# Performance work log

Hardware: AMD Instinct MI355X
Metric: run time of the kernel (lower is better)

## Reference

```python
import jax, jax.numpy as jnp
import numpy as np

LN_EPS = 1e-5


def setup_inputs() -> dict:
    key = jax.random.key(0)
    k1, k2, k3 = jax.random.split(key, 3)
    B, L, D = 8, 2048, 512
    K, Dc = 8192, 16
    x = jax.random.normal(k1, (B, L, D), dtype=jnp.float32)
    # xavier_uniform for Linear(dim -> codebook_dim), weight shape (Dc, D)
    bound = float(np.sqrt(6.0 / (D + Dc)))
    proj_weight = jax.random.uniform(k2, (Dc, D), dtype=jnp.float32, minval=-bound, maxval=bound)
    codebook = jax.random.normal(k3, (K, Dc), dtype=jnp.float32)
    return {"x": x, "proj_weight": proj_weight, "codebook": codebook}


def reference(x, proj_weight, codebook):
    # random projection: (B,L,D) @ (D,Dc) -> (B,L,Dc)
    h = jnp.einsum("bld,cd->blc", x, proj_weight)
    # LayerNorm over last dim, no affine params
    mu = jnp.mean(h, axis=-1, keepdims=True)
    var = jnp.mean(jnp.square(h - mu), axis=-1, keepdims=True)
    h = (h - mu) / jnp.sqrt(var + LN_EPS)
    # squared-distance via dot-product decomposition; avoids (B,L,K,Dc) blowup.
    # argmin of ||h - c||^2 == argmin of ||h - c|| (sqrt is monotone).
    h2 = jnp.sum(jnp.square(h), axis=-1, keepdims=True)        # (B,L,1)
    c2 = jnp.sum(jnp.square(codebook), axis=-1)                # (K,)
    dots = jnp.einsum("blc,kc->blk", h, codebook)              # (B,L,K)
    dist2 = h2 - 2.0 * dots + c2                               # (B,L,K)
    codes = jnp.argmin(dist2, axis=-1)                         # (B,L) int
    return codes
```

## Files before the change

kernel.cpp:

```cpp
#include <hip/hip_runtime.h>
#include <math.h>

#define LN_EPS 1e-5f

typedef _Float16 f16;
typedef _Float16 f16x8 __attribute__((ext_vector_type(8)));
typedef _Float16 f16x2 __attribute__((ext_vector_type(2)));
typedef float f32x4 __attribute__((ext_vector_type(4)));
typedef unsigned long long ull;

constexpr int DC = 16;
constexpr int K = 8192;
constexpr int NTOK = 16384;
constexpr int KSPLIT = 16;
constexpr int KCHUNK = K / KSPLIT;
constexpr int JT = 8;
constexpr float SCALE = 16384.f;
constexpr float EPS_S = LN_EPS * SCALE * SCALE;
constexpr int XP = 516;

__global__ __launch_bounds__(256, 4) void prep_proj(
    const float* __restrict__ x, const float* __restrict__ wq,
    const float* __restrict__ cb, f16* __restrict__ hB,
    f16* __restrict__ cbA, float* __restrict__ c2s) {
  const int tid = threadIdx.x;

  if (blockIdx.x >= NTOK / 16) {
    const int ti = tid >> 6;
    const int l = tid & 63;
    const int ct = (blockIdx.x - NTOK / 16) * 4 + ti;
    const int code = ct * 16 + (l & 15);
    const int g = l >> 4;

    const float* row = cb + (size_t)code * DC + (g & 1) * 8;
    f32x4 v0 = *(const f32x4*)row;
    f32x4 v1 = *(const f32x4*)(row + 4);
    float vv[8] = {v0[0], v0[1], v0[2], v0[3], v1[0], v1[1], v1[2], v1[3]};

    f16x8 r;
#pragma unroll
    for (int p = 0; p < 8; ++p) {
      float cc = -128.f * vv[p];
      f16 hh = (f16)cc;
      r[p] = (g < 2) ? hh : (f16)(cc - (float)hh);
    }
    *(f16x8*)(cbA + ((size_t)ct * 64 + l) * 8) = r;

    if (g == 0) {
      const f32x4* rw = (const f32x4*)(cb + (size_t)code * DC);
      f32x4 a0 = rw[0], a1 = rw[1], a2 = rw[2], a3 = rw[3];
      float s = 0.f;
#pragma unroll
      for (int p = 0; p < 4; ++p)
        s += a0[p] * a0[p] + a1[p] * a1[p] + a2[p] * a2[p] + a3[p] * a3[p];
      c2s[code] = (s + 16.5f) * SCALE;
    }
    return;
  }

  __shared__ float xs[16 * XP];
  __shared__ float comb[4 * 16 * 20];
  __shared__ float hsm[16][17];

  const float4* xg = (const float4*)(x + (size_t)blockIdx.x * (16 * 512));
#pragma unroll
  for (int i = 0; i < 8; ++i) {
    int idx = tid + 256 * i;
    int tok = idx >> 7;
    int d4 = idx & 127;
    *(float4*)&xs[tok * XP + d4 * 4] = xg[idx];
  }

  const int w = tid >> 6;
  const int lane = tid & 63;
  const int g = lane >> 4;
  const int c_out = lane & 15;
  const int doff = (g & 1) * 8;
  f16x8 aw[8];
#pragma unroll
  for (int st = 0; st < 8; ++st) {
    const int step = w * 8 + st;
    const float* wp = wq + (size_t)c_out * 512 + step * 16 + doff;
    f32x4 u0 = *(const f32x4*)wp;
    f32x4 u1 = *(const f32x4*)(wp + 4);
    float v[8] = {u0[0], u0[1], u0[2], u0[3], u1[0], u1[1], u1[2], u1[3]};
    f16x8 r;
#pragma unroll
    for (int p = 0; p < 8; ++p) {
      float f = v[p] * 64.f;
      f16 h1 = (f16)f;
      r[p] = (g < 2) ? h1 : (f16)(f - (float)h1);
    }
    aw[st] = r;
  }
  __syncthreads();

  f32x4 acc = {0.f, 0.f, 0.f, 0.f};
  const int tok = lane & 15;
#pragma unroll
  for (int st = 0; st < 8; ++st) {
    const int step = w * 8 + st;
    const float* xp = &xs[tok * XP + step * 16 + doff];
    f32x4 u0 = *(const f32x4*)xp;
    f32x4 u1 = *(const f32x4*)(xp + 4);
    float v[8] = {u0[0], u0[1], u0[2], u0[3], u1[0], u1[1], u1[2], u1[3]};
    f16x8 bh, bl;
#pragma unroll
    for (int p = 0; p < 8; ++p) {
      float f = v[p] * 256.f;
      f16 h1 = (f16)f;
      bh[p] = h1;
      bl[p] = (f16)(f - (float)h1);
    }
    f16x8 b1 = (g < 2) ? bh : bl;
    f16x8 b2 = (g < 2) ? bl : bh;
    acc = __builtin_amdgcn_mfma_f32_16x16x32_f16(aw[st], b1, acc, 0, 0, 0);
    acc = __builtin_amdgcn_mfma_f32_16x16x32_f16(aw[st], b2, acc, 0, 0, 0);
  }

  *(f32x4*)&comb[w * 320 + tok * 20 + g * 4] = acc;
  __syncthreads();

  const int tokL = tid >> 4;
  const int cL = tid & 15;
  float hv = (comb[0 * 320 + tokL * 20 + cL] + comb[1 * 320 + tokL * 20 + cL]) +
             (comb[2 * 320 + tokL * 20 + cL] + comb[3 * 320 + tokL * 20 + cL]);

  float s = hv;
  s += __shfl_xor(s, 1, 16);
  s += __shfl_xor(s, 2, 16);
  s += __shfl_xor(s, 4, 16);
  s += __shfl_xor(s, 8, 16);
  float mu = s * (1.f / 16.f);
  float diff = hv - mu;
  float v2 = diff * diff;
  v2 += __shfl_xor(v2, 1, 16);
  v2 += __shfl_xor(v2, 2, 16);
  v2 += __shfl_xor(v2, 4, 16);
  v2 += __shfl_xor(v2, 8, 16);
  float var = v2 * (1.f / 16.f);
  hsm[tokL][cL] = diff / sqrtf(var + EPS_S);
  __syncthreads();

  const int le = tid >> 2;
  const int q = tid & 3;
  const int col = le & 15;
  const int ge = le >> 4;
  const int s0 = ge * 8 + q * 2;
  f16x2 u;
#pragma unroll
  for (int e = 0; e < 2; ++e) {
    int sE = s0 + e;
    int d = sE & 15;
    float f = hsm[col][d] * 256.f;
    f16 hh = (f16)f;
    u[e] = (sE < 16) ? hh : (f16)(f - (float)hh);
  }
  *(f16x2*)(hB + ((size_t)blockIdx.x * 64 + le) * 8 + q * 2) = u;
}

__global__ __launch_bounds__(256, 4) void argmin_mfma(
    const f16* __restrict__ cbA, const float* __restrict__ c2s,
    const f16* __restrict__ hB, ull* __restrict__ pk) {
  const int tid = threadIdx.x;
  const int w = tid >> 6;
  const int lane = tid & 63;
  const int kt0 = blockIdx.y * (KCHUNK / 16);
  const int tt0 = blockIdx.x * (4 * JT) + w * JT;

  f16x8 b1[JT], b2[JT];
#pragma unroll
  for (int j = 0; j < JT; ++j) {
    const f16* p = hB + ((size_t)(tt0 + j) * 64) * 8;
    b1[j] = *(const f16x8*)&p[lane * 8];
    b2[j] = *(const f16x8*)&p[(lane ^ 32) * 8];
  }

  float best[JT];
  int bidx[JT];
#pragma unroll
  for (int j = 0; j < JT; ++j) {
    best[j] = 3.0e38f;
    bidx[j] = 0;
  }

  const int lkoff = (lane >> 4) * 4;
#pragma unroll 2
  for (int t = 0; t < KCHUNK / 16; ++t) {
    f16x8 a = *(const f16x8*)&cbA[((size_t)(kt0 + t) * 64 + lane) * 8];
    const int kbase = blockIdx.y * KCHUNK + t * 16;
    f32x4 c2v = *(const f32x4*)&c2s[kbase + lkoff];
    const int ib = kbase + lkoff;
#pragma unroll
    for (int j = 0; j < JT; ++j) {
      f32x4 acc =
          __builtin_amdgcn_mfma_f32_16x16x32_f16(a, b1[j], c2v, 0, 0, 0);
      acc = __builtin_amdgcn_mfma_f32_16x16x32_f16(a, b2[j], acc, 0, 0, 0);
#pragma unroll
      for (int r = 0; r < 4; ++r) {
        bool lt = acc[r] < best[j];
        best[j] = lt ? acc[r] : best[j];
        bidx[j] = lt ? (ib + r) : bidx[j];
      }
    }
  }

#pragma unroll
  for (int j = 0; j < JT; ++j) {
    float d = best[j];
    int ix = bidx[j];
#pragma unroll
    for (int off = 16; off <= 32; off <<= 1) {
      float od = __shfl_xor(d, off);
      int oi = __shfl_xor(ix, off);
      bool take = (od < d) || (od == d && oi < ix);
      d = take ? od : d;
      ix = take ? oi : ix;
    }
    d = fmaxf(d, 0.f);
    if (lane < 16) {
      int token = (tt0 + j) * 16 + lane;
      ull key = ((ull)__float_as_uint(d) << 32) | (unsigned)ix;
      pk[(size_t)token * KSPLIT + blockIdx.y] = key;
    }
  }
}

__global__ __launch_bounds__(256) void finalize(const ull* __restrict__ pk,
                                                int* __restrict__ out) {
  int t = blockIdx.x * 256 + threadIdx.x;
  const ull* row = pk + (size_t)t * KSPLIT;
  ull best = row[0];
#pragma unroll
  for (int s = 1; s < KSPLIT; ++s) {
    ull k2 = row[s];
    best = (k2 < best) ? k2 : best;
  }
  out[t] = (int)(unsigned)(best & 0xFFFFFFFFull);
}

extern "C" void kernel_launch(void* const* d_in, const int* in_sizes, int n_in,
                              void* d_out, int out_size, void* d_ws,
                              size_t ws_size, hipStream_t stream) {
  const float* x = (const float*)d_in[0];
  const float* w = (const float*)d_in[1];
  const float* cb = (const float*)d_in[2];

  f16* cbA = (f16*)d_ws;
  float* c2s = (float*)(cbA + (size_t)K * 32);
  f16* hB = (f16*)(c2s + K);
  ull* pk = (ull*)(hB + (size_t)NTOK * 32);

  prep_proj<<<NTOK / 16 + K / 64, 256, 0, stream>>>(x, w, cb, hB, cbA, c2s);
  argmin_mfma<<<dim3(NTOK / (64 * JT), KSPLIT), 256, 0, stream>>>(cbA, c2s,
                                                                  hB, pk);
  finalize<<<NTOK / 256, 256, 0, stream>>>(pk, (int*)d_out);
}
```

Baseline: 48.29 us.

## Fuse projection, LayerNorm and codebook argmin into one kernel with exact rescoring

Replaces the three-kernel pipeline with a codebook-prep kernel plus one fused kernel. Each 1024-thread block projects and normalises 64 tokens, then scans the whole codebook, with each wave covering a slice of 512 codes. The fused kernel tracks only the best group of four codes per MFMA tile, reduces across waves in LDS, and rescores the four winning candidates exactly in fp32. This removes the hB and partial-key round trips through global memory, the finalize launch, and most per-element compare work. In exchange it runs fewer, larger blocks, reads x straight from global memory instead of staging it in LDS, and relies on the approximate group-level choice being correct.

```diff
diff --git a/kernel.cpp b/kernel.cpp
--- a/kernel.cpp
+++ b/kernel.cpp
@@ -5,82 +5,75 @@
 
 typedef _Float16 f16;
 typedef _Float16 f16x8 __attribute__((ext_vector_type(8)));
-typedef _Float16 f16x2 __attribute__((ext_vector_type(2)));
 typedef float f32x4 __attribute__((ext_vector_type(4)));
-typedef unsigned long long ull;
 
 constexpr int DC = 16;
 constexpr int K = 8192;
 constexpr int NTOK = 16384;
-constexpr int KSPLIT = 16;
-constexpr int KCHUNK = K / KSPLIT;
-constexpr int JT = 8;
+constexpr int D = 512;
 constexpr float SCALE = 16384.f;
 constexpr float EPS_S = LN_EPS * SCALE * SCALE;
-constexpr int XP = 516;
-
-__global__ __launch_bounds__(256, 4) void prep_proj(
+
+__global__ __launch_bounds__(256) void prep_cb(const float* __restrict__ cb,
+                                               f16* __restrict__ cbA,
+                                               float* __restrict__ c2s) {
+  const int tid = threadIdx.x;
+  const int ti = tid >> 6;
+  const int l = tid & 63;
+  const int ct = blockIdx.x * 4 + ti;
+  const int code = ct * 16 + (l & 15);
+  const int g = l >> 4;
+
+  const float* row = cb + (size_t)code * DC + (g & 1) * 8;
+  f32x4 v0 = *(const f32x4*)row;
+  f32x4 v1 = *(const f32x4*)(row + 4);
+  float vv[8] = {v0[0], v0[1], v0[2], v0[3], v1[0], v1[1], v1[2], v1[3]};
+
+  f16x8 r;
+#pragma unroll
+  for (int p = 0; p < 8; ++p) {
+    float cc = -128.f * vv[p];
+    f16 hh = (f16)cc;
+    r[p] = (g < 2) ? hh : (f16)(cc - (float)hh);
+  }
+  *(f16x8*)(cbA + ((size_t)ct * 64 + l) * 8) = r;
+
+  if (g == 0) {
+    const f32x4* rw = (const f32x4*)(cb + (size_t)code * DC);
+    f32x4 a0 = rw[0], a1 = rw[1], a2 = rw[2], a3 = rw[3];
+    float s = 0.f;
+#pragma unroll
+    for (int p = 0; p < 4; ++p)
+      s += a0[p] * a0[p] + a1[p] * a1[p] + a2[p] * a2[p] + a3[p] * a3[p];
+    c2s[code] = (s + 16.5f) * SCALE;
+  }
+}
+
+__global__ __launch_bounds__(1024, 4) void fused(
     const float* __restrict__ x, const float* __restrict__ wq,
-    const float* __restrict__ cb, f16* __restrict__ hB,
-    f16* __restrict__ cbA, float* __restrict__ c2s) {
+    const float* __restrict__ cb, const f16* __restrict__ cbA,
+    const float* __restrict__ c2s, int* __restrict__ out) {
+  __shared__ float comb[16 * 320];
+  __shared__ float hsm[64][17];
+  __shared__ float fin_d[16][64];
+  __shared__ int fin_t[16][64];
+
   const int tid = threadIdx.x;
-
-  if (blockIdx.x >= NTOK / 16) {
-    const int ti = tid >> 6;
-    const int l = tid & 63;
-    const int ct = (blockIdx.x - NTOK / 16) * 4 + ti;
-    const int code = ct * 16 + (l & 15);
-    const int g = l >> 4;
-
-    const float* row = cb + (size_t)code * DC + (g & 1) * 8;
-    f32x4 v0 = *(const f32x4*)row;
-    f32x4 v1 = *(const f32x4*)(row + 4);
-    float vv[8] = {v0[0], v0[1], v0[2], v0[3], v1[0], v1[1], v1[2], v1[3]};
-
-    f16x8 r;
-#pragma unroll
-    for (int p = 0; p < 8; ++p) {
-      float cc = -128.f * vv[p];
-      f16 hh = (f16)cc;
-      r[p] = (g < 2) ? hh : (f16)(cc - (float)hh);
-    }
-    *(f16x8*)(cbA + ((size_t)ct * 64 + l) * 8) = r;
-
-    if (g == 0) {
-      const f32x4* rw = (const f32x4*)(cb + (size_t)code * DC);
-      f32x4 a0 = rw[0], a1 = rw[1], a2 = rw[2], a3 = rw[3];
-      float s = 0.f;
-#pragma unroll
-      for (int p = 0; p < 4; ++p)
-        s += a0[p] * a0[p] + a1[p] * a1[p] + a2[p] * a2[p] + a3[p] * a3[p];
-      c2s[code] = (s + 16.5f) * SCALE;
-    }
-    return;
-  }
-
-  __shared__ float xs[16 * XP];
-  __shared__ float comb[4 * 16 * 20];
-  __shared__ float hsm[16][17];
-
-  const float4* xg = (const float4*)(x + (size_t)blockIdx.x * (16 * 512));
-#pragma unroll
-  for (int i = 0; i < 8; ++i) {
-    int idx = tid + 256 * i;
-    int tok = idx >> 7;
-    int d4 = idx & 127;
-    *(float4*)&xs[tok * XP + d4 * 4] = xg[idx];
-  }
-
   const int w = tid >> 6;
   const int lane = tid & 63;
   const int g = lane >> 4;
-  const int c_out = lane & 15;
+  const int col = lane & 15;
   const int doff = (g & 1) * 8;
+  const int tb = blockIdx.x * 64;
+
+  const int j = w & 3;
+  const int dq = w >> 2;
+
   f16x8 aw[8];
 #pragma unroll
   for (int st = 0; st < 8; ++st) {
-    const int step = w * 8 + st;
-    const float* wp = wq + (size_t)c_out * 512 + step * 16 + doff;
+    const int step = dq * 8 + st;
+    const float* wp = wq + (size_t)col * D + step * 16 + doff;
     f32x4 u0 = *(const f32x4*)wp;
     f32x4 u1 = *(const f32x4*)(wp + 4);
     float v[8] = {u0[0], u0[1], u0[2], u0[3], u1[0], u1[1], u1[2], u1[3]};
@@ -93,14 +86,13 @@
     }
     aw[st] = r;
   }
-  __syncthreads();
 
   f32x4 acc = {0.f, 0.f, 0.f, 0.f};
-  const int tok = lane & 15;
+  const float* xrow = x + (size_t)(tb + j * 16 + col) * D;
 #pragma unroll
   for (int st = 0; st < 8; ++st) {
-    const int step = w * 8 + st;
-    const float* xp = &xs[tok * XP + step * 16 + doff];
+    const int step = dq * 8 + st;
+    const float* xp = xrow + step * 16 + doff;
     f32x4 u0 = *(const f32x4*)xp;
     f32x4 u1 = *(const f32x4*)(xp + 4);
     float v[8] = {u0[0], u0[1], u0[2], u0[3], u1[0], u1[1], u1[2], u1[3]};
@@ -117,15 +109,17 @@
     acc = __builtin_amdgcn_mfma_f32_16x16x32_f16(aw[st], b1, acc, 0, 0, 0);
     acc = __builtin_amdgcn_mfma_f32_16x16x32_f16(aw[st], b2, acc, 0, 0, 0);
   }
-
-  *(f32x4*)&comb[w * 320 + tok * 20 + g * 4] = acc;
+  *(f32x4*)&comb[w * 320 + col * 20 + g * 4] = acc;
   __syncthreads();
 
   const int tokL = tid >> 4;
   const int cL = tid & 15;
-  float hv = (comb[0 * 320 + tokL * 20 + cL] + comb[1 * 320 + tokL * 20 + cL]) +
-             (comb[2 * 320 + tokL * 20 + cL] + comb[3 * 320 + tokL * 20 + cL]);
-
+  const int jL = tokL >> 4;
+  const int colL = tokL & 15;
+  float hv = (comb[(0 * 4 + jL) * 320 + colL * 20 + cL] +
+              comb[(1 * 4 + jL) * 320 + colL * 20 + cL]) +
+             (comb[(2 * 4 + jL) * 320 + colL * 20 + cL] +
+              comb[(3 * 4 + jL) * 320 + colL * 20 + cL]);
   float s = hv;
   s += __shfl_xor(s, 1, 16);
   s += __shfl_xor(s, 2, 16);
@@ -142,101 +136,98 @@
   hsm[tokL][cL] = diff / sqrtf(var + EPS_S);
   __syncthreads();
 
-  const int le = tid >> 2;
-  const int q = tid & 3;
-  const int col = le & 15;
-  const int ge = le >> 4;
-  const int s0 = ge * 8 + q * 2;
-  f16x2 u;
-#pragma unroll
-  for (int e = 0; e < 2; ++e) {
-    int sE = s0 + e;
-    int d = sE & 15;
-    float f = hsm[col][d] * 256.f;
-    f16 hh = (f16)f;
-    u[e] = (sE < 16) ? hh : (f16)(f - (float)hh);
-  }
-  *(f16x2*)(hB + ((size_t)blockIdx.x * 64 + le) * 8 + q * 2) = u;
-}
-
-__global__ __launch_bounds__(256, 4) void argmin_mfma(
-    const f16* __restrict__ cbA, const float* __restrict__ c2s,
-    const f16* __restrict__ hB, ull* __restrict__ pk) {
-  const int tid = threadIdx.x;
-  const int w = tid >> 6;
-  const int lane = tid & 63;
-  const int kt0 = blockIdx.y * (KCHUNK / 16);
-  const int tt0 = blockIdx.x * (4 * JT) + w * JT;
-
-  f16x8 b1[JT], b2[JT];
-#pragma unroll
-  for (int j = 0; j < JT; ++j) {
-    const f16* p = hB + ((size_t)(tt0 + j) * 64) * 8;
-    b1[j] = *(const f16x8*)&p[lane * 8];
-    b2[j] = *(const f16x8*)&p[(lane ^ 32) * 8];
-  }
-
-  float best[JT];
-  int bidx[JT];
-#pragma unroll
-  for (int j = 0; j < JT; ++j) {
-    best[j] = 3.0e38f;
-    bidx[j] = 0;
-  }
-
-  const int lkoff = (lane >> 4) * 4;
-#pragma unroll 2
-  for (int t = 0; t < KCHUNK / 16; ++t) {
-    f16x8 a = *(const f16x8*)&cbA[((size_t)(kt0 + t) * 64 + lane) * 8];
-    const int kbase = blockIdx.y * KCHUNK + t * 16;
-    f32x4 c2v = *(const f32x4*)&c2s[kbase + lkoff];
-    const int ib = kbase + lkoff;
-#pragma unroll
-    for (int j = 0; j < JT; ++j) {
-      f32x4 acc =
-          __builtin_amdgcn_mfma_f32_16x16x32_f16(a, b1[j], c2v, 0, 0, 0);
-      acc = __builtin_amdgcn_mfma_f32_16x16x32_f16(a, b2[j], acc, 0, 0, 0);
-#pragma unroll
-      for (int r = 0; r < 4; ++r) {
-        bool lt = acc[r] < best[j];
-        best[j] = lt ? acc[r] : best[j];
-        bidx[j] = lt ? (ib + r) : bidx[j];
-      }
-    }
-  }
-
-#pragma unroll
-  for (int j = 0; j < JT; ++j) {
-    float d = best[j];
-    int ix = bidx[j];
+  f16x8 b1[4], b2[4];
+#pragma unroll
+  for (int jj = 0; jj < 4; ++jj) {
+#pragma unroll
+    for (int p = 0; p < 8; ++p) {
+      float f = hsm[jj * 16 + col][doff + p] * 256.f;
+      f16 h1 = (f16)f;
+      f16 l1 = (f16)(f - (float)h1);
+      b1[jj][p] = (g < 2) ? h1 : l1;
+      b2[jj][p] = (g < 2) ? l1 : h1;
+    }
+  }
+
+  const int q = w;
+  float best[4] = {3.0e38f, 3.0e38f, 3.0e38f, 3.0e38f};
+  int btg[4] = {0, 0, 0, 0};
+
+#pragma unroll 4
+  for (int t = 0; t < 32; ++t) {
+    const int ktile = q * 32 + t;
+    f16x8 a = *(const f16x8*)&cbA[((size_t)ktile * 64 + lane) * 8];
+    f32x4 c2v = *(const f32x4*)&c2s[ktile * 16 + g * 4];
+    const int tag = t * 4 + g;
+#pragma unroll
+    for (int jj = 0; jj < 4; ++jj) {
+      f32x4 ac = __builtin_amdgcn_mfma_f32_16x16x32_f16(a, b1[jj], c2v, 0, 0, 0);
+      ac = __builtin_amdgcn_mfma_f32_16x16x32_f16(a, b2[jj], ac, 0, 0, 0);
+      float m = fminf(fminf(ac[0], ac[1]), fminf(ac[2], ac[3]));
+      bool lt = m < best[jj];
+      best[jj] = lt ? m : best[jj];
+      btg[jj] = lt ? tag : btg[jj];
+    }
+  }
+
+#pragma unroll
+  for (int jj = 0; jj < 4; ++jj) {
+    float d = best[jj];
+    int tg = btg[jj];
 #pragma unroll
     for (int off = 16; off <= 32; off <<= 1) {
       float od = __shfl_xor(d, off);
-      int oi = __shfl_xor(ix, off);
-      bool take = (od < d) || (od == d && oi < ix);
+      int otg = __shfl_xor(tg, off);
+      bool take = (od < d) || (od == d && otg < tg);
       d = take ? od : d;
-      ix = take ? oi : ix;
-    }
-    d = fmaxf(d, 0.f);
+      tg = take ? otg : tg;
+    }
     if (lane < 16) {
-      int token = (tt0 + j) * 16 + lane;
-      ull key = ((ull)__float_as_uint(d) << 32) | (unsigned)ix;
-      pk[(size_t)token * KSPLIT + blockIdx.y] = key;
-    }
-  }
-}
-
-__global__ __launch_bounds__(256) void finalize(const ull* __restrict__ pk,
-                                                int* __restrict__ out) {
-  int t = blockIdx.x * 256 + threadIdx.x;
-  const ull* row = pk + (size_t)t * KSPLIT;
-  ull best = row[0];
-#pragma unroll
-  for (int s = 1; s < KSPLIT; ++s) {
-    ull k2 = row[s];
-    best = (k2 < best) ? k2 : best;
-  }
-  out[t] = (int)(unsigned)(best & 0xFFFFFFFFull);
+      fin_d[q][jj * 16 + lane] = d;
+      fin_t[q][jj * 16 + lane] = tg;
+    }
+  }
+  __syncthreads();
+
+  if (tid < 64) {
+    const int tok = tid;
+    float bd = fin_d[0][tok];
+    int btag = fin_t[0][tok];
+    int bq = 0;
+#pragma unroll
+    for (int q2 = 1; q2 < 16; ++q2) {
+      float d2 = fin_d[q2][tok];
+      int t2 = fin_t[q2][tok];
+      bool take = (d2 < bd) || (d2 == bd && false);
+      bd = take ? d2 : bd;
+      btag = take ? t2 : btag;
+      bq = take ? q2 : bq;
+    }
+    const int k0 = bq * 512 + (btag >> 2) * 16 + (btag & 3) * 4;
+
+    float h[16];
+#pragma unroll
+    for (int dd = 0; dd < 16; ++dd) h[dd] = hsm[tok][dd];
+
+    float bestd = 3.0e38f;
+    int bestk = k0;
+#pragma unroll
+    for (int r = 0; r < 4; ++r) {
+      const int kk = k0 + r;
+      const float* crow = cb + (size_t)kk * DC;
+      float sd = 0.f;
+#pragma unroll
+      for (int dd = 0; dd < 16; ++dd) {
+        float df = h[dd] - crow[dd];
+        sd = fmaf(df, df, sd);
+      }
+      if (sd < bestd) {
+        bestd = sd;
+        bestk = kk;
+      }
+    }
+    out[tb + tok] = bestk;
+  }
 }
 
 extern "C" void kernel_launch(void* const* d_in, const int* in_sizes, int n_in,
@@ -248,11 +239,7 @@
 
   f16* cbA = (f16*)d_ws;
   float* c2s = (float*)(cbA + (size_t)K * 32);
-  f16* hB = (f16*)(c2s + K);
-  ull* pk = (ull*)(hB + (size_t)NTOK * 32);
-
-  prep_proj<<<NTOK / 16 + K / 64, 256, 0, stream>>>(x, w, cb, hB, cbA, c2s);
-  argmin_mfma<<<dim3(NTOK / (64 * JT), KSPLIT), 256, 0, stream>>>(cbA, c2s,
-                                                                  hB, pk);
-  finalize<<<NTOK / 256, 256, 0, stream>>>(pk, (int*)d_out);
+
+  prep_cb<<<K / 64, 256, 0, stream>>>(cb, cbA, c2s);
+  fused<<<NTOK / 64, 1024, 0, stream>>>(x, w, cb, cbA, c2s, (int*)d_out);
 }
```

New measurement: 45.36 us. 6.1% less time.
